# Optimization experiments

Hardware: AMD Instinct MI355X
Metric: run time of the kernel (lower is better)

The kernel has to match this reference:

```python
import jax, jax.numpy as jnp
import numpy as np

HEADS = 16
DIM_HEAD = 64
EPS = 1e-8


def setup_inputs() -> dict:
    key = jax.random.key(0)
    ks = jax.random.split(key, 5)
    B, N, D = 2, 2048, 1024
    inner = HEADS * DIM_HEAD
    return {
        "x": jax.random.normal(ks[0], (B, N, D), jnp.float32),
        "Wq": jax.random.normal(ks[1], (D, inner), jnp.float32) * (D ** -0.5),
        "Wkv": jax.random.normal(ks[2], (D, 2 * inner), jnp.float32) * (D ** -0.5),
        "Wo": jax.random.normal(ks[3], (inner, D), jnp.float32) * (inner ** -0.5),
        "bo": jax.random.normal(ks[4], (D,), jnp.float32) * 0.02,
    }


def reference(x, Wq, Wkv, Wo, bo):
    # Self-attention (context = x), causal, memory-efficient path.
    # The chunked online-softmax in the source is mathematically equivalent to:
    #   gm = rowwise max of raw (unmasked) scores (stop-gradient, as in .detach())
    #   p  = exp(s - gm) with causal-masked entries zeroed (exp(-finfo.max) == 0)
    #   out = (p @ v) / (sum_j p + eps)
    B, N, D = x.shape
    H, Dh = HEADS, DIM_HEAD
    scale = Dh ** -0.5

    q = (x @ Wq).reshape(B, N, H, Dh).transpose(0, 2, 1, 3)  # b h n d
    kv = x @ Wkv
    k = kv[..., : H * Dh].reshape(B, N, H, Dh).transpose(0, 2, 1, 3)
    v = kv[..., H * Dh :].reshape(B, N, H, Dh).transpose(0, 2, 1, 3)

    s = jnp.einsum("bhid,bhjd->bhij", q * scale, k)  # b h i j
    gm = jax.lax.stop_gradient(jnp.max(s, axis=-1, keepdims=True))
    causal_mask = jnp.triu(jnp.ones((N, N), bool), 1)  # True above diagonal -> masked
    p = jnp.where(causal_mask, 0.0, jnp.exp(s - gm))
    num = jnp.einsum("bhij,bhjd->bhid", p, v)
    out = num / (jnp.sum(p, axis=-1, keepdims=True) + EPS)  # b h n d

    out = out.transpose(0, 2, 1, 3).reshape(B, N, H * Dh)  # b n (h d)
    return out @ Wo + bo
```

## Files before the change

### kernel.cpp

```cpp
#include <hip/hip_runtime.h>

typedef _Float16 f16;
typedef __attribute__((ext_vector_type(8))) _Float16 f16x8;
typedef __attribute__((ext_vector_type(4))) _Float16 f16x4;
typedef __attribute__((ext_vector_type(4))) float   f32x4;

typedef unsigned int u32;
typedef __attribute__((address_space(1))) const u32 gu32;
typedef __attribute__((address_space(3))) u32 lu32;

__device__ inline void gll16(const void* g, void* l) {
  __builtin_amdgcn_global_load_lds((gu32*)g, (lu32*)l, 16, 0, 0);
}

__global__ void prep(const float* __restrict__ Wq, const float* __restrict__ Wkv,
                     const float* __restrict__ Wo, const float* __restrict__ x,
                     f16* __restrict__ WqkvT, f16* __restrict__ WoT, f16* __restrict__ xb) {
  __shared__ float tile[32][33];
  int z = blockIdx.z;
  int tx = threadIdx.x, ty = threadIdx.y;
  if (z == 3) {
    size_t flat = ((size_t)(blockIdx.y * 64 + blockIdx.x) * 256 + ty * 32 + tx) * 2;
    for (int i = 0; i < 2; i++) {
      float4 v = ((const float4*)x)[flat + i];
      f16x4 r = { (f16)v.x, (f16)v.y, (f16)v.z, (f16)v.w };
      ((f16x4*)xb)[flat + i] = r;
    }
    return;
  }
  const float* src; f16* dst; int W;
  if (z == 0)      { src = Wq;  dst = WqkvT;                       W = 1024; }
  else if (z == 1) { src = Wkv; dst = WqkvT + (size_t)1024 * 1024; W = 2048; }
  else             { src = Wo;  dst = WoT;                         W = 1024; }
  int c0 = blockIdx.x * 32, r0 = blockIdx.y * 32;
  if (c0 >= W) return;
  for (int i = 0; i < 4; i++)
    tile[ty + i * 8][tx] = src[(size_t)(r0 + ty + i * 8) * W + c0 + tx];
  __syncthreads();
  for (int i = 0; i < 4; i++)
    dst[(size_t)(c0 + ty + i * 8) * 1024 + r0 + tx] = (f16)tile[tx][ty + i * 8];
}

__global__ __launch_bounds__(256) void gemm1(
    const f16* __restrict__ A, const f16* __restrict__ Bt,
    f16* __restrict__ qb, f16* __restrict__ kb, f16* __restrict__ vtb) {
  const int K = 1024;
  __shared__ f16 As[128 * 32];
  __shared__ f16 Bs[128 * 32];
  int tid = threadIdx.x;
  int wave = tid >> 6, lane = tid & 63, quad = lane >> 4, l16 = lane & 15;
  int m0 = blockIdx.y * 128, n0 = blockIdx.x * 128;
  int wr = (wave >> 1) * 64, wc = (wave & 1) * 64;

  f32x4 acc[4][4] = {};

  int gA = (((lane & 3) ^ ((lane >> 3) & 3))) * 8;
  const f16* Ag = A  + (size_t)(m0 + wave * 32 + (lane >> 2)) * K + gA;
  const f16* Bg = Bt + (size_t)(n0 + wave * 32 + (lane >> 2)) * K + gA;
  f16* Asw = As + wave * 1024;
  f16* Bsw = Bs + wave * 1024;
  int rsz = (l16 >> 1) & 3;

  for (int k0 = 0; k0 < K; k0 += 32) {
    gll16(Ag + k0, Asw);
    gll16(Ag + (size_t)16 * K + k0, Asw + 512);
    gll16(Bg + k0, Bsw);
    gll16(Bg + (size_t)16 * K + k0, Bsw + 512);
    __syncthreads();
    f16x8 af[4], bf[4];
    for (int mt = 0; mt < 4; mt++)
      af[mt] = *(const f16x8*)&As[(wr + mt * 16 + l16) * 32 + ((quad ^ rsz) << 3)];
    for (int nt = 0; nt < 4; nt++)
      bf[nt] = *(const f16x8*)&Bs[(wc + nt * 16 + l16) * 32 + ((quad ^ rsz) << 3)];
    for (int mt = 0; mt < 4; mt++)
      for (int nt = 0; nt < 4; nt++)
        acc[mt][nt] = __builtin_amdgcn_mfma_f32_16x16x32_f16(af[mt], bf[nt], acc[mt][nt], 0, 0, 0);
    __syncthreads();
  }

  if (n0 < 2048) {
    for (int mt = 0; mt < 4; mt++)
      for (int nt = 0; nt < 4; nt++)
        for (int r = 0; r < 4; r++) {
          int row = m0 + wr + mt * 16 + quad * 4 + r;
          int col = n0 + wc + nt * 16 + l16;
          float v = acc[mt][nt][r];
          int b = row >> 11, n = row & 2047;
          if (col < 1024) {
            qb[(((size_t)b * 16 + (col >> 6)) * 2048 + n) * 64 + (col & 63)] =
                (f16)(v * 0.1803368801111137f);
          } else {
            int c = col - 1024;
            kb[(((size_t)b * 16 + (c >> 6)) * 2048 + n) * 64 + (c & 63)] = (f16)v;
          }
        }
  } else {
    for (int mt = 0; mt < 4; mt++)
      for (int nt = 0; nt < 4; nt++) {
        int rb = m0 + wr + mt * 16 + quad * 4;
        int c  = n0 + wc + nt * 16 + l16 - 2048;
        int b = rb >> 11, n = rb & 2047;
        f16x4 pk = { (f16)acc[mt][nt][0], (f16)acc[mt][nt][1],
                     (f16)acc[mt][nt][2], (f16)acc[mt][nt][3] };
        size_t idx = (((size_t)(b * 16 + (c >> 6)) * 32 + (n >> 6)) * 64 + (c & 63)) * 64 + (n & 63);
        *(f16x4*)&vtb[idx] = pk;
      }
  }
}

__global__ __launch_bounds__(256) void gemm2(
    const f16* __restrict__ A, const f16* __restrict__ Bt,
    const float* __restrict__ bo, float* __restrict__ outf) {
  const int K = 1024;
  __shared__ f16 As[128 * 32];
  __shared__ f16 Bs[64 * 32];
  int tid = threadIdx.x;
  int wave = tid >> 6, lane = tid & 63, quad = lane >> 4, l16 = lane & 15;
  int m0 = blockIdx.y * 128, n0 = blockIdx.x * 64;
  int wr = (wave >> 1) * 64, wc = (wave & 1) * 32;

  f32x4 acc[4][2] = {};

  int gA = (((lane & 3) ^ ((lane >> 3) & 3))) * 8;
  const f16* Ag = A  + (size_t)(m0 + wave * 32 + (lane >> 2)) * K + gA;
  const f16* Bg = Bt + (size_t)(n0 + wave * 16 + (lane >> 2)) * K + gA;
  f16* Asw = As + wave * 1024;
  f16* Bsw = Bs + wave * 512;
  int rsz = (l16 >> 1) & 3;

  for (int k0 = 0; k0 < K; k0 += 32) {
    gll16(Ag + k0, Asw);
    gll16(Ag + (size_t)16 * K + k0, Asw + 512);
    gll16(Bg + k0, Bsw);
    __syncthreads();
    f16x8 af[4], bf[2];
    for (int mt = 0; mt < 4; mt++)
      af[mt] = *(const f16x8*)&As[(wr + mt * 16 + l16) * 32 + ((quad ^ rsz) << 3)];
    for (int nt = 0; nt < 2; nt++)
      bf[nt] = *(const f16x8*)&Bs[(wc + nt * 16 + l16) * 32 + ((quad ^ rsz) << 3)];
    for (int mt = 0; mt < 4; mt++)
      for (int nt = 0; nt < 2; nt++)
        acc[mt][nt] = __builtin_amdgcn_mfma_f32_16x16x32_f16(af[mt], bf[nt], acc[mt][nt], 0, 0, 0);
    __syncthreads();
  }

  for (int mt = 0; mt < 4; mt++)
    for (int nt = 0; nt < 2; nt++)
      for (int r = 0; r < 4; r++) {
        int row = m0 + wr + mt * 16 + quad * 4 + r;
        int col = n0 + wc + nt * 16 + l16;
        outf[(size_t)row * 1024 + col] = acc[mt][nt][r] + bo[col];
      }
}

__global__ __launch_bounds__(256, 4) void attn(
    const f16* __restrict__ qb, const f16* __restrict__ kb,
    const f16* __restrict__ vtb, f16* __restrict__ ob) {
  __shared__ f16 Ks[64 * 64];
  __shared__ f16 Vs[64 * 64];
  __shared__ f16 Ps[4][16 * 64];
  int tid = threadIdx.x, wave = tid >> 6, lane = tid & 63, quad = lane >> 4, l16 = lane & 15;
  int l7 = l16 & 7;

  int bx = blockIdx.x;
  int q = bx >> 8, r = bx & 255;
  int xcd = r & 7, idx = r >> 3;
  int bh = xcd * 4 + (idx & 3);
  int srem = idx >> 2;
  int t;
  if (q == 0)      t = srem;
  else if (q == 1) t = 15 - srem;
  else if (q == 2) t = 16 + srem;
  else             t = 31 - srem;
  int qi0 = t * 64;
  int b = bh >> 4, h = bh & 15;

  const f16* Q  = qb + (size_t)bh * 2048 * 64;
  const char* Kg = (const char*)(kb + (size_t)bh * 2048 * 64);
  const char* Vbase = (const char*)(vtb + (size_t)bh * 32 * 4096);
  int wq0 = qi0 + wave * 16;
  int i = wq0 + l16;

  f16x8 qf[2];
  for (int ks = 0; ks < 2; ks++)
    qf[ks] = *(const f16x8*)&Q[(size_t)(wq0 + l16) * 64 + ks * 32 + quad * 8];

  f32x4 acc[4] = {};
  float mrow = -1e30f, lrow = 0.f;

  int sg = ((lane & 7) ^ ((lane >> 3) & 7)) * 16;
  int jl = wave * 16 + (lane >> 3);

  for (int j0 = 0; j0 < qi0 + 64; j0 += 64) {
    const char* kg = Kg + (size_t)j0 * 128;
    const char* vt = Vbase + (size_t)(j0 >> 6) * 8192;
    gll16(kg + (size_t)jl * 128 + sg,        (char*)Ks + wave * 2048);
    gll16(kg + (size_t)(jl + 8) * 128 + sg,  (char*)Ks + wave * 2048 + 1024);
    gll16(vt + (size_t)jl * 128 + sg,        (char*)Vs + wave * 2048);
    gll16(vt + (size_t)(jl + 8) * 128 + sg,  (char*)Vs + wave * 2048 + 1024);
    __syncthreads();

    if (j0 <= wq0 + 15) {
      f16x8 kf[4][2], vf[4][2];
      for (int nt = 0; nt < 4; nt++)
        for (int ks = 0; ks < 2; ks++) {
          int pos = ((ks * 4 + quad) ^ l7) << 3;
          kf[nt][ks] = *(const f16x8*)&Ks[(nt * 16 + l16) * 64 + pos];
          vf[nt][ks] = *(const f16x8*)&Vs[(nt * 16 + l16) * 64 + pos];
        }

      f32x4 st[4];
      for (int nt = 0; nt < 4; nt++) {
        f32x4 z = {0.f, 0.f, 0.f, 0.f};
        z = __builtin_amdgcn_mfma_f32_16x16x32_f16(kf[nt][0], qf[0], z, 0, 0, 0);
        z = __builtin_amdgcn_mfma_f32_16x16x32_f16(kf[nt][1], qf[1], z, 0, 0, 0);
        st[nt] = z;
      }
      if (j0 + 63 > wq0) {
        for (int nt = 0; nt < 4; nt++) {
          int jc = j0 + nt * 16 + quad * 4;
          for (int rr = 0; rr < 4; rr++)
            st[nt][rr] = (jc + rr <= i) ? st[nt][rr] : -1e30f;
        }
      }
      float v = fmaxf(fmaxf(fmaxf(st[0][0], st[0][1]), fmaxf(st[0][2], st[0][3])),
                      fmaxf(fmaxf(st[1][0], st[1][1]), fmaxf(st[1][2], st[1][3])));
      v = fmaxf(v, fmaxf(fmaxf(fmaxf(st[2][0], st[2][1]), fmaxf(st[2][2], st[2][3])),
                         fmaxf(fmaxf(st[3][0], st[3][1]), fmaxf(st[3][2], st[3][3]))));
      v = fmaxf(v, __shfl_xor(v, 16));
      v = fmaxf(v, __shfl_xor(v, 32));
      float mold = mrow;
      float mn = fmaxf(mold, v);
      mrow = mn;
      if (__any(mn > mold)) {
        float al = __builtin_amdgcn_exp2f(mold - mn);
        lrow *= al;
        for (int nt = 0; nt < 4; nt++)
          for (int rr = 0; rr < 4; rr++) acc[nt][rr] *= al;
      }
      float psum = 0.f;
      for (int nt = 0; nt < 4; nt++) {
        f16x4 pk;
        for (int rr = 0; rr < 4; rr++) {
          float p = __builtin_amdgcn_exp2f(st[nt][rr] - mn);
          psum += p;
          pk[rr] = (f16)p;
        }
        int pos = (nt * 2 + (quad >> 1)) ^ l7;
        *(f16x4*)((char*)&Ps[wave][0] + l16 * 128 + pos * 16 + (quad & 1) * 8) = pk;
      }
      psum += __shfl_xor(psum, 16);
      psum += __shfl_xor(psum, 32);
      lrow += psum;

      for (int ks = 0; ks < 2; ks++) {
        f16x8 pf = *(const f16x8*)((char*)&Ps[wave][0] + l16 * 128 + (((ks * 4 + quad) ^ l7) * 16));
        for (int nt = 0; nt < 4; nt++)
          acc[nt] = __builtin_amdgcn_mfma_f32_16x16x32_f16(vf[nt][ks], pf, acc[nt], 0, 0, 0);
      }
    }
    __syncthreads();
  }

  float inv = 1.f / (lrow + 1e-8f);
  int n = wq0 + l16;
  for (int nt = 0; nt < 4; nt++) {
    f16x4 o = { (f16)(acc[nt][0] * inv), (f16)(acc[nt][1] * inv),
                (f16)(acc[nt][2] * inv), (f16)(acc[nt][3] * inv) };
    *(f16x4*)&ob[((size_t)b * 2048 + n) * 1024 + h * 64 + nt * 16 + quad * 4] = o;
  }
}

extern "C" void kernel_launch(void* const* d_in, const int* in_sizes, int n_in,
                              void* d_out, int out_size, void* d_ws, size_t ws_size,
                              hipStream_t stream) {
  const float* x   = (const float*)d_in[0];
  const float* Wq  = (const float*)d_in[1];
  const float* Wkv = (const float*)d_in[2];
  const float* Wo  = (const float*)d_in[3];
  const float* bo  = (const float*)d_in[4];
  float* out = (float*)d_out;

  char* ws = (char*)d_ws;
  f16* xb    = (f16*)ws;  ws += (size_t)4096 * 1024 * 2;
  f16* WqkvT = (f16*)ws;  ws += (size_t)3072 * 1024 * 2;
  f16* WoT   = (f16*)ws;  ws += (size_t)1024 * 1024 * 2;
  f16* qb    = (f16*)ws;  ws += (size_t)32 * 2048 * 64 * 2;
  f16* kb    = (f16*)ws;  ws += (size_t)32 * 2048 * 64 * 2;
  f16* vtb   = (f16*)ws;  ws += (size_t)32 * 64 * 2048 * 2;
  f16* ob    = xb;

  prep<<<dim3(64, 32, 4), dim3(32, 8), 0, stream>>>(Wq, Wkv, Wo, x, WqkvT, WoT, xb);
  gemm1<<<dim3(24, 32), 256, 0, stream>>>(xb, WqkvT, qb, kb, vtb);
  attn<<<dim3(1024), 256, 0, stream>>>(qb, kb, vtb, ob);
  gemm2<<<dim3(16, 32), 256, 0, stream>>>(ob, WoT, bo, out);
}
```

Before: 180.4 us.

## Split causal attention across KV chunks with a combine pass; deepen GEMM K-tiles

```diff
diff --git a/kernel.cpp b/kernel.cpp
--- a/kernel.cpp
+++ b/kernel.cpp
@@ -45,36 +45,39 @@
     const f16* __restrict__ A, const f16* __restrict__ Bt,
     f16* __restrict__ qb, f16* __restrict__ kb, f16* __restrict__ vtb) {
   const int K = 1024;
-  __shared__ f16 As[128 * 32];
-  __shared__ f16 Bs[128 * 32];
+  __shared__ f16 As[128 * 64];
+  __shared__ f16 Bs[128 * 64];
   int tid = threadIdx.x;
   int wave = tid >> 6, lane = tid & 63, quad = lane >> 4, l16 = lane & 15;
+  int l7 = l16 & 7;
   int m0 = blockIdx.y * 128, n0 = blockIdx.x * 128;
   int wr = (wave >> 1) * 64, wc = (wave & 1) * 64;
 
   f32x4 acc[4][4] = {};
 
-  int gA = (((lane & 3) ^ ((lane >> 3) & 3))) * 8;
-  const f16* Ag = A  + (size_t)(m0 + wave * 32 + (lane >> 2)) * K + gA;
-  const f16* Bg = Bt + (size_t)(n0 + wave * 32 + (lane >> 2)) * K + gA;
-  f16* Asw = As + wave * 1024;
-  f16* Bsw = Bs + wave * 1024;
-  int rsz = (l16 >> 1) & 3;
-
-  for (int k0 = 0; k0 < K; k0 += 32) {
-    gll16(Ag + k0, Asw);
-    gll16(Ag + (size_t)16 * K + k0, Asw + 512);
-    gll16(Bg + k0, Bsw);
-    gll16(Bg + (size_t)16 * K + k0, Bsw + 512);
-    __syncthreads();
-    f16x8 af[4], bf[4];
-    for (int mt = 0; mt < 4; mt++)
-      af[mt] = *(const f16x8*)&As[(wr + mt * 16 + l16) * 32 + ((quad ^ rsz) << 3)];
-    for (int nt = 0; nt < 4; nt++)
-      bf[nt] = *(const f16x8*)&Bs[(wc + nt * 16 + l16) * 32 + ((quad ^ rsz) << 3)];
-    for (int mt = 0; mt < 4; mt++)
+  int swz = ((lane & 7) ^ ((lane >> 3) & 7)) * 8;
+  const f16* Ag = A  + (size_t)(m0 + wave * 32 + (lane >> 3)) * K + swz;
+  const f16* Bg = Bt + (size_t)(n0 + wave * 32 + (lane >> 3)) * K + swz;
+  f16* Asw = As + wave * 2048;
+  f16* Bsw = Bs + wave * 2048;
+
+  for (int k0 = 0; k0 < K; k0 += 64) {
+    for (int q = 0; q < 4; q++) {
+      gll16(Ag + k0 + (size_t)q * 8 * K, Asw + q * 512);
+      gll16(Bg + k0 + (size_t)q * 8 * K, Bsw + q * 512);
+    }
+    __syncthreads();
+    for (int ks = 0; ks < 2; ks++) {
+      int pos = ((ks * 4 + quad) ^ l7) * 8;
+      f16x8 af[4], bf[4];
+      for (int mt = 0; mt < 4; mt++)
+        af[mt] = *(const f16x8*)&As[(wr + mt * 16 + l16) * 64 + pos];
       for (int nt = 0; nt < 4; nt++)
-        acc[mt][nt] = __builtin_amdgcn_mfma_f32_16x16x32_f16(af[mt], bf[nt], acc[mt][nt], 0, 0, 0);
+        bf[nt] = *(const f16x8*)&Bs[(wc + nt * 16 + l16) * 64 + pos];
+      for (int mt = 0; mt < 4; mt++)
+        for (int nt = 0; nt < 4; nt++)
+          acc[mt][nt] = __builtin_amdgcn_mfma_f32_16x16x32_f16(af[mt], bf[nt], acc[mt][nt], 0, 0, 0);
+    }
     __syncthreads();
   }
 
@@ -112,35 +115,39 @@
     const f16* __restrict__ A, const f16* __restrict__ Bt,
     const float* __restrict__ bo, float* __restrict__ outf) {
   const int K = 1024;
-  __shared__ f16 As[128 * 32];
-  __shared__ f16 Bs[64 * 32];
+  __shared__ f16 As[128 * 64];
+  __shared__ f16 Bs[64 * 64];
   int tid = threadIdx.x;
   int wave = tid >> 6, lane = tid & 63, quad = lane >> 4, l16 = lane & 15;
+  int l7 = l16 & 7;
   int m0 = blockIdx.y * 128, n0 = blockIdx.x * 64;
   int wr = (wave >> 1) * 64, wc = (wave & 1) * 32;
 
   f32x4 acc[4][2] = {};
 
-  int gA = (((lane & 3) ^ ((lane >> 3) & 3))) * 8;
-  const f16* Ag = A  + (size_t)(m0 + wave * 32 + (lane >> 2)) * K + gA;
-  const f16* Bg = Bt + (size_t)(n0 + wave * 16 + (lane >> 2)) * K + gA;
-  f16* Asw = As + wave * 1024;
-  f16* Bsw = Bs + wave * 512;
-  int rsz = (l16 >> 1) & 3;
-
-  for (int k0 = 0; k0 < K; k0 += 32) {
-    gll16(Ag + k0, Asw);
-    gll16(Ag + (size_t)16 * K + k0, Asw + 512);
+  int swz = ((lane & 7) ^ ((lane >> 3) & 7)) * 8;
+  const f16* Ag = A  + (size_t)(m0 + wave * 32 + (lane >> 3)) * K + swz;
+  const f16* Bg = Bt + (size_t)(n0 + wave * 16 + (lane >> 3)) * K + swz;
+  f16* Asw = As + wave * 2048;
+  f16* Bsw = Bs + wave * 1024;
+
+  for (int k0 = 0; k0 < K; k0 += 64) {
+    for (int q = 0; q < 4; q++)
+      gll16(Ag + k0 + (size_t)q * 8 * K, Asw + q * 512);
     gll16(Bg + k0, Bsw);
-    __syncthreads();
-    f16x8 af[4], bf[2];
-    for (int mt = 0; mt < 4; mt++)
-      af[mt] = *(const f16x8*)&As[(wr + mt * 16 + l16) * 32 + ((quad ^ rsz) << 3)];
-    for (int nt = 0; nt < 2; nt++)
-      bf[nt] = *(const f16x8*)&Bs[(wc + nt * 16 + l16) * 32 + ((quad ^ rsz) << 3)];
-    for (int mt = 0; mt < 4; mt++)
+    gll16(Bg + k0 + (size_t)8 * K, Bsw + 512);
+    __syncthreads();
+    for (int ks = 0; ks < 2; ks++) {
+      int pos = ((ks * 4 + quad) ^ l7) * 8;
+      f16x8 af[4], bf[2];
+      for (int mt = 0; mt < 4; mt++)
+        af[mt] = *(const f16x8*)&As[(wr + mt * 16 + l16) * 64 + pos];
       for (int nt = 0; nt < 2; nt++)
-        acc[mt][nt] = __builtin_amdgcn_mfma_f32_16x16x32_f16(af[mt], bf[nt], acc[mt][nt], 0, 0, 0);
+        bf[nt] = *(const f16x8*)&Bs[(wc + nt * 16 + l16) * 64 + pos];
+      for (int mt = 0; mt < 4; mt++)
+        for (int nt = 0; nt < 2; nt++)
+          acc[mt][nt] = __builtin_amdgcn_mfma_f32_16x16x32_f16(af[mt], bf[nt], acc[mt][nt], 0, 0, 0);
+    }
     __syncthreads();
   }
 
@@ -153,27 +160,27 @@
       }
 }
 
-__global__ __launch_bounds__(256, 4) void attn(
+__global__ __launch_bounds__(256, 6) void attn(
     const f16* __restrict__ qb, const f16* __restrict__ kb,
-    const f16* __restrict__ vtb, f16* __restrict__ ob) {
+    const f16* __restrict__ vtb, f16* __restrict__ PO,
+    float* __restrict__ PM, float* __restrict__ PL) {
   __shared__ f16 Ks[64 * 64];
   __shared__ f16 Vs[64 * 64];
   __shared__ f16 Ps[4][16 * 64];
   int tid = threadIdx.x, wave = tid >> 6, lane = tid & 63, quad = lane >> 4, l16 = lane & 15;
-  int l7 = l16 & 7;
+  int l7 = l16 & 15 & 7;
 
   int bx = blockIdx.x;
-  int q = bx >> 8, r = bx & 255;
-  int xcd = r & 7, idx = r >> 3;
-  int bh = xcd * 4 + (idx & 3);
-  int srem = idx >> 2;
-  int t;
-  if (q == 0)      t = srem;
-  else if (q == 1) t = 15 - srem;
-  else if (q == 2) t = 16 + srem;
-  else             t = 31 - srem;
+  int bh = (bx & 7) * 4 + ((bx >> 3) & 3);
+  int task = bx >> 5;
+  int t, c;
+  if (task < 8)       { t = task;                          c = 0; }
+  else if (task < 24) { int u = task - 8;  t = 8 + (u >> 1);  c = u & 1; }
+  else if (task < 48) { int u = task - 24; t = 16 + u / 3;    c = u % 3; }
+  else                { int u = task - 48; t = 24 + (u >> 2); c = u & 3; }
   int qi0 = t * 64;
-  int b = bh >> 4, h = bh & 15;
+  int jlo = c * 512;
+  int jhi = min(jlo + 512, qi0 + 64);
 
   const f16* Q  = qb + (size_t)bh * 2048 * 64;
   const char* Kg = (const char*)(kb + (size_t)bh * 2048 * 64);
@@ -191,7 +198,7 @@
   int sg = ((lane & 7) ^ ((lane >> 3) & 7)) * 16;
   int jl = wave * 16 + (lane >> 3);
 
-  for (int j0 = 0; j0 < qi0 + 64; j0 += 64) {
+  for (int j0 = jlo; j0 < jhi; j0 += 64) {
     const char* kg = Kg + (size_t)j0 * 128;
     const char* vt = Vbase + (size_t)(j0 >> 6) * 8192;
     gll16(kg + (size_t)jl * 128 + sg,        (char*)Ks + wave * 2048);
@@ -262,12 +269,52 @@
     __syncthreads();
   }
 
-  float inv = 1.f / (lrow + 1e-8f);
-  int n = wq0 + l16;
-  for (int nt = 0; nt < 4; nt++) {
-    f16x4 o = { (f16)(acc[nt][0] * inv), (f16)(acc[nt][1] * inv),
-                (f16)(acc[nt][2] * inv), (f16)(acc[nt][3] * inv) };
-    *(f16x4*)&ob[((size_t)b * 2048 + n) * 1024 + h * 64 + nt * 16 + quad * 4] = o;
+  size_t pb = ((size_t)bh * 80 + task) * 4096;
+  int it = wave * 16 + l16;
+  for (int nt = 0; nt < 4; nt++)
+    for (int rr = 0; rr < 4; rr++)
+      PO[pb + (size_t)(nt * 16 + quad * 4 + rr) * 64 + it] = (f16)acc[nt][rr];
+  if (quad == 0) {
+    PM[(size_t)(bh * 80 + task) * 64 + it] = mrow;
+    PL[(size_t)(bh * 80 + task) * 64 + it] = lrow;
+  }
+}
+
+__global__ __launch_bounds__(256) void combine(
+    const f16* __restrict__ PO, const float* __restrict__ PM,
+    const float* __restrict__ PL, f16* __restrict__ ob) {
+  int bx = blockIdx.x;
+  int bh = bx & 31, t = bx >> 5;
+  int b = bh >> 4, h = bh & 15;
+  int nc = (t + 8) >> 3;
+  int base = (t < 8) ? t : (t < 16) ? 8 + 2 * (t - 8)
+           : (t < 24) ? 24 + 3 * (t - 16) : 48 + 4 * (t - 24);
+  int tid = threadIdx.x;
+  int i = tid & 63, dg = tid >> 6;
+
+  size_t tb = (size_t)bh * 80 + base;
+  float m[4], w[4];
+  float gm = -1e30f;
+  for (int c = 0; c < nc; c++) { m[c] = PM[(tb + c) * 64 + i]; gm = fmaxf(gm, m[c]); }
+  float l = 0.f;
+  for (int c = 0; c < nc; c++) {
+    w[c] = __builtin_amdgcn_exp2f(m[c] - gm);
+    l += w[c] * PL[(tb + c) * 64 + i];
+  }
+  float inv = 1.f / (l + 1e-8f);
+
+  float Ov[16] = {};
+  for (int c = 0; c < nc; c++) {
+    const f16* po = PO + (tb + c) * 4096 + (size_t)dg * 16 * 64 + i;
+    float wc = w[c];
+    for (int dd = 0; dd < 16; dd++)
+      Ov[dd] += wc * (float)po[dd * 64];
+  }
+  f16* dst = &ob[((size_t)b * 2048 + t * 64 + i) * 1024 + h * 64 + dg * 16];
+  for (int g = 0; g < 4; g++) {
+    f16x4 o = { (f16)(Ov[g * 4] * inv), (f16)(Ov[g * 4 + 1] * inv),
+                (f16)(Ov[g * 4 + 2] * inv), (f16)(Ov[g * 4 + 3] * inv) };
+    *(f16x4*)&dst[g * 4] = o;
   }
 }
 
@@ -288,10 +335,14 @@
   f16* qb    = (f16*)ws;  ws += (size_t)32 * 2048 * 64 * 2;
   f16* kb    = (f16*)ws;  ws += (size_t)32 * 2048 * 64 * 2;
   f16* vtb   = (f16*)ws;  ws += (size_t)32 * 64 * 2048 * 2;
+  f16* PO    = (f16*)ws;  ws += (size_t)32 * 80 * 4096 * 2;
+  float* PM  = (float*)ws; ws += (size_t)32 * 80 * 64 * 4;
+  float* PL  = (float*)ws; ws += (size_t)32 * 80 * 64 * 4;
   f16* ob    = xb;
 
   prep<<<dim3(64, 32, 4), dim3(32, 8), 0, stream>>>(Wq, Wkv, Wo, x, WqkvT, WoT, xb);
   gemm1<<<dim3(24, 32), 256, 0, stream>>>(xb, WqkvT, qb, kb, vtb);
-  attn<<<dim3(1024), 256, 0, stream>>>(qb, kb, vtb, ob);
+  attn<<<dim3(2560), 256, 0, stream>>>(qb, kb, vtb, PO, PM, PL);
+  combine<<<dim3(1024), 256, 0, stream>>>(PO, PM, PL, ob);
   gemm2<<<dim3(16, 32), 256, 0, stream>>>(ob, WoT, bo, out);
 }
```

Result: slower. 275.1 us (+52.5%).

## Split causal key blocks across waves in attention and merge partials via LDS

Applied to the files above, without the earlier changes.

```diff
diff --git a/kernel.cpp b/kernel.cpp
--- a/kernel.cpp
+++ b/kernel.cpp
@@ -153,12 +153,10 @@
       }
 }
 
-__global__ __launch_bounds__(256, 4) void attn(
+__global__ __launch_bounds__(256, 2) void attn(
     const f16* __restrict__ qb, const f16* __restrict__ kb,
     const f16* __restrict__ vtb, f16* __restrict__ ob) {
-  __shared__ f16 Ks[64 * 64];
-  __shared__ f16 Vs[64 * 64];
-  __shared__ f16 Ps[4][16 * 64];
+  __shared__ __align__(16) char SMEM[75776];
   int tid = threadIdx.x, wave = tid >> 6, lane = tid & 63, quad = lane >> 4, l16 = lane & 15;
   int l7 = l16 & 7;
 
@@ -167,56 +165,66 @@
   int xcd = r & 7, idx = r >> 3;
   int bh = xcd * 4 + (idx & 3);
   int srem = idx >> 2;
-  int t;
-  if (q == 0)      t = srem;
-  else if (q == 1) t = 15 - srem;
-  else if (q == 2) t = 16 + srem;
-  else             t = 31 - srem;
+  int t = (q == 0) ? srem : (q == 1) ? 15 - srem : (q == 2) ? 16 + srem : 31 - srem;
   int qi0 = t * 64;
   int b = bh >> 4, h = bh & 15;
+  int T = t + 1, C = (T + 3) >> 2;
 
   const f16* Q  = qb + (size_t)bh * 2048 * 64;
   const char* Kg = (const char*)(kb + (size_t)bh * 2048 * 64);
   const char* Vbase = (const char*)(vtb + (size_t)bh * 32 * 4096);
-  int wq0 = qi0 + wave * 16;
-  int i = wq0 + l16;
-
-  f16x8 qf[2];
-  for (int ks = 0; ks < 2; ks++)
-    qf[ks] = *(const f16x8*)&Q[(size_t)(wq0 + l16) * 64 + ks * 32 + quad * 8];
-
-  f32x4 acc[4] = {};
-  float mrow = -1e30f, lrow = 0.f;
+
+  f16* Kw = (f16*)(SMEM + wave * 16384);
+  f16* Vw = Kw + 4096;
+  f16* Pw = (f16*)(SMEM + 65536 + wave * 2048);
+  float* Msp = (float*)(SMEM + 73728);
+  float* Lsp = (float*)(SMEM + 74752);
+
+  f16x8 qf[4][2];
+  for (int mt = 0; mt < 4; mt++)
+    for (int ks = 0; ks < 2; ks++)
+      qf[mt][ks] = *(const f16x8*)&Q[(size_t)(qi0 + mt * 16 + l16) * 64 + ks * 32 + quad * 8];
+
+  f32x4 acc[4][4] = {};
+  float mrow[4], lrow[4];
+  for (int mt = 0; mt < 4; mt++) { mrow[mt] = -1e30f; lrow[mt] = 0.f; }
 
   int sg = ((lane & 7) ^ ((lane >> 3) & 7)) * 16;
-  int jl = wave * 16 + (lane >> 3);
-
-  for (int j0 = 0; j0 < qi0 + 64; j0 += 64) {
+
+  for (int n = 0; n < C; n++) {
+    int jb = wave * C + n;
+    if (jb >= T) break;
+    int j0 = jb * 64;
     const char* kg = Kg + (size_t)j0 * 128;
     const char* vt = Vbase + (size_t)(j0 >> 6) * 8192;
-    gll16(kg + (size_t)jl * 128 + sg,        (char*)Ks + wave * 2048);
-    gll16(kg + (size_t)(jl + 8) * 128 + sg,  (char*)Ks + wave * 2048 + 1024);
-    gll16(vt + (size_t)jl * 128 + sg,        (char*)Vs + wave * 2048);
-    gll16(vt + (size_t)(jl + 8) * 128 + sg,  (char*)Vs + wave * 2048 + 1024);
-    __syncthreads();
-
-    if (j0 <= wq0 + 15) {
-      f16x8 kf[4][2], vf[4][2];
-      for (int nt = 0; nt < 4; nt++)
-        for (int ks = 0; ks < 2; ks++) {
-          int pos = ((ks * 4 + quad) ^ l7) << 3;
-          kf[nt][ks] = *(const f16x8*)&Ks[(nt * 16 + l16) * 64 + pos];
-          vf[nt][ks] = *(const f16x8*)&Vs[(nt * 16 + l16) * 64 + pos];
-        }
+    for (int qq = 0; qq < 8; qq++)
+      gll16(kg + (size_t)(qq * 8 + (lane >> 3)) * 128 + sg, (char*)Kw + qq * 1024);
+    for (int qq = 0; qq < 8; qq++)
+      gll16(vt + (size_t)(qq * 8 + (lane >> 3)) * 128 + sg, (char*)Vw + qq * 1024);
+
+    __builtin_amdgcn_s_waitcnt(0x0F78);
+    f16x8 kf[4][2];
+    for (int nt = 0; nt < 4; nt++)
+      for (int ks = 0; ks < 2; ks++)
+        kf[nt][ks] = *(const f16x8*)&Kw[(nt * 16 + l16) * 64 + (((ks * 4 + quad) ^ l7) << 3)];
+    __builtin_amdgcn_s_waitcnt(0x0F70);
+    f16x8 vf[4][2];
+    for (int nt = 0; nt < 4; nt++)
+      for (int ks = 0; ks < 2; ks++)
+        vf[nt][ks] = *(const f16x8*)&Vw[(nt * 16 + l16) * 64 + (((ks * 4 + quad) ^ l7) << 3)];
+
+    bool last = (j0 == qi0);
+    for (int mt = 0; mt < 4; mt++) {
+      int i = qi0 + mt * 16 + l16;
 
       f32x4 st[4];
       for (int nt = 0; nt < 4; nt++) {
         f32x4 z = {0.f, 0.f, 0.f, 0.f};
-        z = __builtin_amdgcn_mfma_f32_16x16x32_f16(kf[nt][0], qf[0], z, 0, 0, 0);
-        z = __builtin_amdgcn_mfma_f32_16x16x32_f16(kf[nt][1], qf[1], z, 0, 0, 0);
+        z = __builtin_amdgcn_mfma_f32_16x16x32_f16(kf[nt][0], qf[mt][0], z, 0, 0, 0);
+        z = __builtin_amdgcn_mfma_f32_16x16x32_f16(kf[nt][1], qf[mt][1], z, 0, 0, 0);
         st[nt] = z;
       }
-      if (j0 + 63 > wq0) {
+      if (last) {
         for (int nt = 0; nt < 4; nt++) {
           int jc = j0 + nt * 16 + quad * 4;
           for (int rr = 0; rr < 4; rr++)
@@ -229,14 +237,14 @@
                          fmaxf(fmaxf(st[3][0], st[3][1]), fmaxf(st[3][2], st[3][3]))));
       v = fmaxf(v, __shfl_xor(v, 16));
       v = fmaxf(v, __shfl_xor(v, 32));
-      float mold = mrow;
+      float mold = mrow[mt];
       float mn = fmaxf(mold, v);
-      mrow = mn;
+      mrow[mt] = mn;
       if (__any(mn > mold)) {
         float al = __builtin_amdgcn_exp2f(mold - mn);
-        lrow *= al;
+        lrow[mt] *= al;
         for (int nt = 0; nt < 4; nt++)
-          for (int rr = 0; rr < 4; rr++) acc[nt][rr] *= al;
+          for (int rr = 0; rr < 4; rr++) acc[mt][nt][rr] *= al;
       }
       float psum = 0.f;
       for (int nt = 0; nt < 4; nt++) {
@@ -247,28 +255,57 @@
           pk[rr] = (f16)p;
         }
         int pos = (nt * 2 + (quad >> 1)) ^ l7;
-        *(f16x4*)((char*)&Ps[wave][0] + l16 * 128 + pos * 16 + (quad & 1) * 8) = pk;
+        *(f16x4*)((char*)Pw + l16 * 128 + pos * 16 + (quad & 1) * 8) = pk;
       }
       psum += __shfl_xor(psum, 16);
       psum += __shfl_xor(psum, 32);
-      lrow += psum;
+      lrow[mt] += psum;
 
       for (int ks = 0; ks < 2; ks++) {
-        f16x8 pf = *(const f16x8*)((char*)&Ps[wave][0] + l16 * 128 + (((ks * 4 + quad) ^ l7) * 16));
+        f16x8 pf = *(const f16x8*)((char*)Pw + l16 * 128 + (((ks * 4 + quad) ^ l7) * 16));
         for (int nt = 0; nt < 4; nt++)
-          acc[nt] = __builtin_amdgcn_mfma_f32_16x16x32_f16(vf[nt][ks], pf, acc[nt], 0, 0, 0);
+          acc[mt][nt] = __builtin_amdgcn_mfma_f32_16x16x32_f16(vf[nt][ks], pf, acc[mt][nt], 0, 0, 0);
       }
     }
-    __syncthreads();
-  }
-
-  float inv = 1.f / (lrow + 1e-8f);
-  int n = wq0 + l16;
-  for (int nt = 0; nt < 4; nt++) {
-    f16x4 o = { (f16)(acc[nt][0] * inv), (f16)(acc[nt][1] * inv),
-                (f16)(acc[nt][2] * inv), (f16)(acc[nt][3] * inv) };
-    *(f16x4*)&ob[((size_t)b * 2048 + n) * 1024 + h * 64 + nt * 16 + quad * 4] = o;
-  }
+  }
+
+  f16* Ow = (f16*)(SMEM + wave * 16384);
+  for (int mt = 0; mt < 4; mt++)
+    for (int nt = 0; nt < 4; nt++) {
+      f16x4 pk = { (f16)acc[mt][nt][0], (f16)acc[mt][nt][1],
+                   (f16)acc[mt][nt][2], (f16)acc[mt][nt][3] };
+      *(f16x4*)((char*)Ow + (mt * 16 + l16) * 144 + (nt * 16 + quad * 4) * 2) = pk;
+    }
+  if (quad == 0)
+    for (int mt = 0; mt < 4; mt++) {
+      Msp[wave * 64 + mt * 16 + l16] = mrow[mt];
+      Lsp[wave * 64 + mt * 16 + l16] = lrow[mt];
+    }
+  __syncthreads();
+
+  int i0 = tid >> 2, db = (tid & 3) * 16;
+  float mw[4], ww[4];
+  float gm = -1e30f;
+  for (int w = 0; w < 4; w++) { mw[w] = Msp[w * 64 + i0]; gm = fmaxf(gm, mw[w]); }
+  float l = 0.f;
+  for (int w = 0; w < 4; w++) {
+    ww[w] = __builtin_amdgcn_exp2f(mw[w] - gm);
+    l += ww[w] * Lsp[w * 64 + i0];
+  }
+  float inv = 1.f / (l + 1e-8f);
+  float Ov[16] = {};
+  for (int w = 0; w < 4; w++) {
+    const f16* Op = (const f16*)((char*)SMEM + w * 16384 + i0 * 144 + db * 2);
+    f16x8 a = *(const f16x8*)Op;
+    f16x8 c = *(const f16x8*)(Op + 8);
+    float wc = ww[w];
+    for (int dd = 0; dd < 8; dd++) { Ov[dd] += wc * (float)a[dd]; Ov[8 + dd] += wc * (float)c[dd]; }
+  }
+  f16* dst = &ob[((size_t)b * 2048 + qi0 + i0) * 1024 + h * 64 + db];
+  f16x8 o1, o2;
+  for (int dd = 0; dd < 8; dd++) { o1[dd] = (f16)(Ov[dd] * inv); o2[dd] = (f16)(Ov[8 + dd] * inv); }
+  *(f16x8*)dst = o1;
+  *(f16x8*)(dst + 8) = o2;
 }
 
 extern "C" void kernel_launch(void* const* d_in, const int* in_sizes, int n_in,
```

After: 181.8 us. Within noise of the previous version (+0.7%).
